# Optimization experiments

Hardware: AMD Instinct MI355X
Metric: run time of the kernel (lower is better)

The kernel has to match this reference:

```python
import jax, jax.numpy as jnp
import numpy as np

N = 50000
E = 800000
F_IN = 64
F_OUT = 64


def setup_inputs() -> dict:
    key = jax.random.key(0)
    ks = jax.random.split(key, 14)
    x = jax.random.normal(ks[0], (N, F_IN), dtype=jnp.float32)
    row_low = jax.random.randint(ks[1], (E,), 0, N)
    col_low = jax.random.randint(ks[2], (E,), 0, N)
    val_low = jax.random.uniform(ks[3], (E,), dtype=jnp.float32)
    row_high = jax.random.randint(ks[4], (E,), 0, N)
    col_high = jax.random.randint(ks[5], (E,), 0, N)
    val_high = jax.random.uniform(ks[6], (E,), dtype=jnp.float32)
    # xavier-uniform style init for weights
    def xavier(k, shape):
        fan_in, fan_out = shape[0], shape[1]
        bound = float(np.sqrt(6.0 / (fan_in + fan_out)))
        return jax.random.uniform(k, shape, jnp.float32, -bound, bound)
    W_low = xavier(ks[7], (F_IN, F_OUT))
    W_high = xavier(ks[8], (F_IN, F_OUT))
    W_mlp = xavier(ks[9], (F_IN, F_OUT))
    a_low = xavier(ks[10], (F_OUT, 1))
    a_high = xavier(ks[11], (F_OUT, 1))
    a_mlp = xavier(ks[12], (F_OUT, 1))
    att3 = xavier(ks[13], (3, 3))
    return dict(x=x, row_low=row_low, col_low=col_low, val_low=val_low,
                row_high=row_high, col_high=col_high, val_high=val_high,
                W_low=W_low, W_high=W_high, W_mlp=W_mlp,
                a_low=a_low, a_high=a_high, a_mlp=a_mlp, att3=att3)


def _spmm(row, col, val, h, n):
    # (sparse adj) @ h : gather source rows, scale by edge weight, scatter-add to dest
    return jax.ops.segment_sum(val[:, None] * h[col], row, num_segments=n)


def reference(x, row_low, col_low, val_low, row_high, col_high, val_high,
              W_low, W_high, W_mlp, a_low, a_high, a_mlp, att3):
    n = x.shape[0]
    out_low = jax.nn.relu(_spmm(row_low, col_low, val_low, x @ W_low, n))
    out_high = jax.nn.relu(_spmm(row_high, col_high, val_high, x @ W_high, n))
    out_mlp = jax.nn.relu(x @ W_mlp)
    T = 3.0
    feats = jnp.concatenate([out_low @ a_low, out_high @ a_high, out_mlp @ a_mlp], axis=1)  # [N,3]
    logits = (jax.nn.sigmoid(feats) @ att3) / T
    att = jax.nn.softmax(logits, axis=1)  # [N,3]
    return 3.0 * (att[:, 0:1] * out_low + att[:, 1:2] * out_high + att[:, 2:3] * out_mlp)
```

## Files before the change

### kernel.cpp

```cpp
#include <hip/hip_runtime.h>


#define NNODE 50000
#define NEDGE 800000
#define NBUCK 782
#define CAP   1300

typedef __attribute__((ext_vector_type(8))) short short8v;
typedef __attribute__((ext_vector_type(4))) float float4v;

__device__ __forceinline__ unsigned short f2bf(float f) {
    unsigned u = __float_as_uint(f);
    u += 0x7FFFu + ((u >> 16) & 1u);
    return (unsigned short)(u >> 16);
}

__global__ __launch_bounds__(256)
void gemm_mfma_kernel(const float* __restrict__ x,
                      const float* __restrict__ Wl, const float* __restrict__ Wh,
                      const float* __restrict__ Wm,
                      unsigned short* __restrict__ hl16,
                      unsigned short* __restrict__ hh16,
                      unsigned short* __restrict__ hm16)
{
    __shared__ unsigned short wt[3][64][72];
    const int t = threadIdx.x;
#pragma unroll 1
    for (int m = 0; m < 3; ++m) {
        const float* __restrict__ W = (m == 0) ? Wl : (m == 1) ? Wh : Wm;
        for (int i = t; i < 4096; i += 256) {
            const int k = i >> 6, c = i & 63;
            wt[m][c][k] = f2bf(W[i]);
        }
    }
    __syncthreads();

    const int wid = t >> 6, lane = t & 63;
    const int node0 = blockIdx.x * 64 + wid * 16;
    if (node0 >= NNODE) return;
    const int arow = lane & 15;
    const int hi = lane >> 4;

    const float* __restrict__ xr = x + (size_t)(node0 + arow) * 64 + hi * 8;
    const float4 pa0 = *(const float4*)(xr + 0);
    const float4 pa1 = *(const float4*)(xr + 4);
    const float4 pb0 = *(const float4*)(xr + 32);
    const float4 pb1 = *(const float4*)(xr + 36);
    short8v a0, a1;
    a0[0] = (short)f2bf(pa0.x); a0[1] = (short)f2bf(pa0.y);
    a0[2] = (short)f2bf(pa0.z); a0[3] = (short)f2bf(pa0.w);
    a0[4] = (short)f2bf(pa1.x); a0[5] = (short)f2bf(pa1.y);
    a0[6] = (short)f2bf(pa1.z); a0[7] = (short)f2bf(pa1.w);
    a1[0] = (short)f2bf(pb0.x); a1[1] = (short)f2bf(pb0.y);
    a1[2] = (short)f2bf(pb0.z); a1[3] = (short)f2bf(pb0.w);
    a1[4] = (short)f2bf(pb1.x); a1[5] = (short)f2bf(pb1.y);
    a1[6] = (short)f2bf(pb1.z); a1[7] = (short)f2bf(pb1.w);

#pragma unroll 1
    for (int m = 0; m < 3; ++m) {
        unsigned short* __restrict__ H = (m == 0) ? hl16 : (m == 1) ? hh16 : hm16;
        float4v acc0 = {0.f, 0.f, 0.f, 0.f}, acc1 = {0.f, 0.f, 0.f, 0.f};
        float4v acc2 = {0.f, 0.f, 0.f, 0.f}, acc3 = {0.f, 0.f, 0.f, 0.f};

#define DO_CT(CT, ACC)                                                          \
        {                                                                       \
            const short8v b0 = *(const short8v*)&wt[m][CT * 16 + arow][hi * 8]; \
            const short8v b1 = *(const short8v*)&wt[m][CT * 16 + arow][32 + hi * 8]; \
            ACC = __builtin_amdgcn_mfma_f32_16x16x32_bf16(a0, b0, ACC, 0, 0, 0); \
            ACC = __builtin_amdgcn_mfma_f32_16x16x32_bf16(a1, b1, ACC, 0, 0, 0); \
        }
        DO_CT(0, acc0) DO_CT(1, acc1) DO_CT(2, acc2) DO_CT(3, acc3)
#undef DO_CT

        const bool rl = (m == 2);
#define ST_CT(CT, ACC)                                                          \
        {                                                                       \
            _Pragma("unroll")                                                   \
            for (int r = 0; r < 4; ++r) {                                       \
                float v = ACC[r];                                               \
                if (rl) v = fmaxf(v, 0.f);                                      \
                H[(size_t)(node0 + hi * 4 + r) * 64 + CT * 16 + arow] = f2bf(v); \
            }                                                                   \
        }
        ST_CT(0, acc0) ST_CT(1, acc1) ST_CT(2, acc2) ST_CT(3, acc3)
#undef ST_CT
    }
}

__global__ __launch_bounds__(512)
void scatter_kernel(const int* __restrict__ row_low, const int* __restrict__ col_low,
                    const float* __restrict__ val_low,
                    const int* __restrict__ row_high, const int* __restrict__ col_high,
                    const float* __restrict__ val_high,
                    unsigned int* __restrict__ gcursor, uint2* __restrict__ packed)
{
    __shared__ unsigned int hist_s[2 * NBUCK];
    __shared__ unsigned int base_s[2 * NBUCK];
    const int t = threadIdx.x;
    const int ebase = blockIdx.x * 8192;

    for (int i = t; i < 2 * NBUCK; i += 512) hist_s[i] = 0u;
    __syncthreads();

    int rows[16]; unsigned int rank[16];
#pragma unroll
    for (int j = 0; j < 16; ++j) {
        const int e = ebase + j * 512 + t;
        rows[j] = 0; rank[j] = 0u;
        if (e < 2 * NEDGE) {
            const int r = (e < NEDGE) ? row_low[e] : row_high[e - NEDGE];
            const int fb = ((e < NEDGE) ? 0 : NBUCK) + (r >> 6);
            rows[j] = r;
            rank[j] = atomicAdd(&hist_s[fb], 1u);
        }
    }
    __syncthreads();
    for (int i = t; i < 2 * NBUCK; i += 512) {
        const unsigned int c = hist_s[i];
        base_s[i] = c ? atomicAdd(&gcursor[i], c) : 0u;
    }
    __syncthreads();
#pragma unroll
    for (int j = 0; j < 16; ++j) {
        const int e = ebase + j * 512 + t;
        if (e < 2 * NEDGE) {
            const int g = (e >= NEDGE);
            const int ee = e - g * NEDGE;
            const int r = rows[j];
            const int c = g ? col_high[ee] : col_low[ee];
            const float v = g ? val_high[ee] : val_low[ee];
            const int fb = g * NBUCK + (r >> 6);
            const unsigned int pos = base_s[fb] + rank[j];
            if (pos < CAP) {
                uint2 pk;
                pk.x = (unsigned int)c | ((unsigned int)(r & 63) << 16);
                pk.y = __float_as_uint(v);
                packed[(size_t)fb * CAP + pos] = pk;
            }
        }
    }
}

__global__ __launch_bounds__(256)
void sort_kernel(uint2* __restrict__ packed,
                 const unsigned int* __restrict__ gcursor,
                 int* __restrict__ rs, int* __restrict__ rc)
{
    __shared__ uint2 es[CAP];
    __shared__ unsigned int hist[64];
    __shared__ unsigned int offs[64];
    __shared__ unsigned int cur[64];

    const int fb = blockIdx.x;
    const int t = threadIdx.x;
    uint2* __restrict__ seg = packed + (size_t)fb * CAP;
    int cnt = (int)gcursor[fb];
    if (cnt > CAP) cnt = CAP;

    if (t < 64) { hist[t] = 0u; cur[t] = 0u; }
    __syncthreads();

    for (int i = t; i < cnt; i += 256) {
        const uint2 p = seg[i];
        es[i] = p;
        atomicAdd(&hist[(p.x >> 16) & 63u], 1u);
    }
    __syncthreads();

    if (t < 64) {
        const int v = (int)hist[t];
        int xsc = v;
#pragma unroll
        for (int d = 1; d < 64; d <<= 1) {
            int y = __shfl_up(xsc, d, 64);
            if (t >= d) xsc += y;
        }
        offs[t] = (unsigned)(xsc - v);
    }
    __syncthreads();

    for (int i = t; i < cnt; i += 256) {
        const uint2 p = es[i];
        const unsigned r = (p.x >> 16) & 63u;
        const unsigned pos = offs[r] + atomicAdd(&cur[r], 1u);
        seg[pos] = p;
    }

    if (t < 64) {
        const int g = (fb >= NBUCK);
        const int node = ((fb - g * NBUCK) << 6) + t;
        if (node < NNODE) {
            rs[g * NNODE + node] = fb * CAP + (int)offs[t];
            rc[g * NNODE + node] = (int)hist[t];
        }
    }
}

#define Q_ISSUE(r0_, r1_, r2_, r3_, rem_, hgp_, U_, V_)                        \
    {                                                                          \
        const unsigned cw = (sub == 0 ? r0_.x : sub == 1 ? r1_.x               \
                             : sub == 2 ? r2_.x : r3_.x);                      \
        const unsigned vb = (sub == 0 ? r0_.y : sub == 1 ? r1_.y               \
                             : sub == 2 ? r2_.y : r3_.y);                      \
        const bool ok = sub < (rem_);                                          \
        const unsigned boff = ok ? ((cw & 0xFFFFu) * 128u + fb2) : fb2;        \
        U_ = *(const uint2*)((const char*)(hgp_) + boff);                      \
        V_ = ok ? __uint_as_float(vb) : 0.f;                                   \
    }

#define Q_FMA(U_, V_, AX_, AY_, AZ_, AW_)                                      \
    {                                                                          \
        AX_ = fmaf(V_, __uint_as_float(U_.x << 16), AX_);                      \
        AY_ = fmaf(V_, __uint_as_float(U_.x & 0xFFFF0000u), AY_);              \
        AZ_ = fmaf(V_, __uint_as_float(U_.y << 16), AZ_);                      \
        AW_ = fmaf(V_, __uint_as_float(U_.y & 0xFFFF0000u), AW_);              \
    }

__global__ __launch_bounds__(256, 4)
void spmm_finalize_kernel(const uint2* __restrict__ packed,
                          const int* __restrict__ rs, const int* __restrict__ rc,
                          const unsigned short* __restrict__ hl16,
                          const unsigned short* __restrict__ hh16,
                          const unsigned short* __restrict__ hm16,
                          const float* __restrict__ aL, const float* __restrict__ aH,
                          const float* __restrict__ aM, const float* __restrict__ att3,
                          float* __restrict__ out)
{
    const int wid = threadIdx.x >> 6;
    const int lane = threadIdx.x & 63;
    const int sub = lane >> 4;
    const int f4 = (lane & 15) << 2;
    const unsigned fb2 = (unsigned)(f4 * 2);
    const int node = blockIdx.x * 4 + wid;
    if (node >= NNODE) return;

    const int sL = __builtin_amdgcn_readfirstlane(rs[node]);
    const int cL = __builtin_amdgcn_readfirstlane(rc[node]);
    const int sH = __builtin_amdgcn_readfirstlane(rs[NNODE + node]);
    const int cH = __builtin_amdgcn_readfirstlane(rc[NNODE + node]);
    const uint2* __restrict__ segL = packed + sL;
    const uint2* __restrict__ segH = packed + sH;
    const int cmax = (cL > cH) ? cL : cH;

    float lx = 0.f, ly = 0.f, lz = 0.f, lw = 0.f;
    float hx = 0.f, hy = 0.f, hz = 0.f, hw = 0.f;

#pragma unroll 1
    for (int i = 0; i < cmax; i += 8) {
        const uint2 l0 = segL[i + 0], l1 = segL[i + 1], l2 = segL[i + 2], l3 = segL[i + 3];
        const uint2 l4 = segL[i + 4], l5 = segL[i + 5], l6 = segL[i + 6], l7 = segL[i + 7];
        const uint2 h0 = segH[i + 0], h1 = segH[i + 1], h2 = segH[i + 2], h3 = segH[i + 3];
        const uint2 h4 = segH[i + 4], h5 = segH[i + 5], h6 = segH[i + 6], h7 = segH[i + 7];
        const int remL = cL - i, remH = cH - i;
        uint2 uL0, uL1, uH0, uH1;
        float vL0, vL1, vH0, vH1;
        Q_ISSUE(l0, l1, l2, l3, remL,     hl16, uL0, vL0);
        Q_ISSUE(l4, l5, l6, l7, remL - 4, hl16, uL1, vL1);
        Q_ISSUE(h0, h1, h2, h3, remH,     hh16, uH0, vH0);
        Q_ISSUE(h4, h5, h6, h7, remH - 4, hh16, uH1, vH1);
        __builtin_amdgcn_sched_barrier(0);
        Q_FMA(uL0, vL0, lx, ly, lz, lw);
        Q_FMA(uL1, vL1, lx, ly, lz, lw);
        Q_FMA(uH0, vH0, hx, hy, hz, hw);
        Q_FMA(uH1, vH1, hx, hy, hz, hw);
    }

    lx += __shfl_xor(lx, 16, 64); ly += __shfl_xor(ly, 16, 64);
    lz += __shfl_xor(lz, 16, 64); lw += __shfl_xor(lw, 16, 64);
    hx += __shfl_xor(hx, 16, 64); hy += __shfl_xor(hy, 16, 64);
    hz += __shfl_xor(hz, 16, 64); hw += __shfl_xor(hw, 16, 64);
    lx += __shfl_xor(lx, 32, 64); ly += __shfl_xor(ly, 32, 64);
    lz += __shfl_xor(lz, 32, 64); lw += __shfl_xor(lw, 32, 64);
    hx += __shfl_xor(hx, 32, 64); hy += __shfl_xor(hy, 32, 64);
    hz += __shfl_xor(hz, 32, 64); hw += __shfl_xor(hw, 32, 64);

    const float olx = fmaxf(lx, 0.f), oly = fmaxf(ly, 0.f);
    const float olz = fmaxf(lz, 0.f), olw = fmaxf(lw, 0.f);
    const float ohx = fmaxf(hx, 0.f), ohy = fmaxf(hy, 0.f);
    const float ohz = fmaxf(hz, 0.f), ohw = fmaxf(hw, 0.f);

    const uint2 om2 = *(const uint2*)&hm16[(size_t)node * 64 + f4];
    const float omx = __uint_as_float(om2.x << 16);
    const float omy = __uint_as_float(om2.x & 0xFFFF0000u);
    const float omz = __uint_as_float(om2.y << 16);
    const float omw = __uint_as_float(om2.y & 0xFFFF0000u);

    const float4 aL4 = *(const float4*)&aL[f4];
    const float4 aH4 = *(const float4*)&aH[f4];
    const float4 aM4 = *(const float4*)&aM[f4];

    float f0 = olx * aL4.x + oly * aL4.y + olz * aL4.z + olw * aL4.w;
    float f1 = ohx * aH4.x + ohy * aH4.y + ohz * aH4.z + ohw * aH4.w;
    float f2 = omx * aM4.x + omy * aM4.y + omz * aM4.z + omw * aM4.w;
#pragma unroll
    for (int msk = 1; msk < 16; msk <<= 1) {
        f0 += __shfl_xor(f0, msk, 64);
        f1 += __shfl_xor(f1, msk, 64);
        f2 += __shfl_xor(f2, msk, 64);
    }
    const float s0 = 1.f / (1.f + __expf(-f0));
    const float s1 = 1.f / (1.f + __expf(-f1));
    const float s2 = 1.f / (1.f + __expf(-f2));
    const float invT = 1.f / 3.f;
    const float l0g = (s0 * att3[0] + s1 * att3[3] + s2 * att3[6]) * invT;
    const float l1g = (s0 * att3[1] + s1 * att3[4] + s2 * att3[7]) * invT;
    const float l2g = (s0 * att3[2] + s1 * att3[5] + s2 * att3[8]) * invT;
    const float mx = fmaxf(l0g, fmaxf(l1g, l2g));
    const float e0 = __expf(l0g - mx);
    const float e1 = __expf(l1g - mx);
    const float e2 = __expf(l2g - mx);
    const float inv = 1.f / (e0 + e1 + e2);
    const float wl = 3.f * inv * e0, wh = 3.f * inv * e1, wm = 3.f * inv * e2;

    if (lane < 16) {
        float4 o;
        o.x = wl * olx + wh * ohx + wm * omx;
        o.y = wl * oly + wh * ohy + wm * omy;
        o.z = wl * olz + wh * ohz + wm * omz;
        o.w = wl * olw + wh * ohw + wm * omw;
        *(float4*)&out[(size_t)node * 64 + f4] = o;
    }
}

extern "C" void kernel_launch(void* const* d_in, const int* in_sizes, int n_in,
                              void* d_out, int out_size, void* d_ws, size_t ws_size,
                              hipStream_t stream)
{
    const float* x        = (const float*)d_in[0];
    const int*   row_low  = (const int*)  d_in[1];
    const int*   col_low  = (const int*)  d_in[2];
    const float* val_low  = (const float*)d_in[3];
    const int*   row_high = (const int*)  d_in[4];
    const int*   col_high = (const int*)  d_in[5];
    const float* val_high = (const float*)d_in[6];
    const float* W_low    = (const float*)d_in[7];
    const float* W_high   = (const float*)d_in[8];
    const float* W_mlp    = (const float*)d_in[9];
    const float* a_low    = (const float*)d_in[10];
    const float* a_high   = (const float*)d_in[11];
    const float* a_mlp    = (const float*)d_in[12];
    const float* att3     = (const float*)d_in[13];
    float* out = (float*)d_out;

    const size_t NM = (size_t)NNODE * 64;

    unsigned short* hl16    = (unsigned short*)d_ws;
    unsigned short* hh16    = hl16 + NM;
    unsigned short* hm16    = hh16 + NM;
    uint2*          packed  = (uint2*)(hm16 + NM);
    unsigned int*   gcursor = (unsigned int*)(packed + (size_t)2 * NBUCK * CAP);
    int*            rs      = (int*)(gcursor + 2 * NBUCK);
    int*            rc      = rs + 2 * NNODE;

    hipMemsetAsync(gcursor, 0, 2 * NBUCK * sizeof(unsigned int), stream);

    scatter_kernel<<<(2 * NEDGE + 8191) / 8192, 512, 0, stream>>>(
        row_low, col_low, val_low, row_high, col_high, val_high, gcursor, packed);

    gemm_mfma_kernel<<<(NNODE + 63) / 64, 256, 0, stream>>>(
        x, W_low, W_high, W_mlp, hl16, hh16, hm16);

    sort_kernel<<<2 * NBUCK, 256, 0, stream>>>(packed, gcursor, rs, rc);

    spmm_finalize_kernel<<<(NNODE + 3) / 4, 256, 0, stream>>>(
        packed, rs, rc, hl16, hh16, hm16, a_low, a_high, a_mlp, att3, out);
}
```

Baseline: 92.34 us.

## Pad per-node edge segments to multiples of eight to simplify SpMM gather loop

The sort kernel now pads each destination node's edge segment to a multiple of eight entries, zero-filling the tail, and stores a quad count instead of a raw edge count. The finalize loop then reads only the one packed entry each 16-lane group needs instead of loading all eight and selecting, which cuts redundant packed loads and selection logic. The launch bound is raised to allow more waves per SIMD, and the memset is replaced with a tiny zero kernel. CAP grows to hold the padding, and entries past CAP are dropped, which risks lost edges for overfull buckets.

```diff
diff --git a/kernel.cpp b/kernel.cpp
--- a/kernel.cpp
+++ b/kernel.cpp
@@ -4,7 +4,7 @@
 #define NNODE 50000
 #define NEDGE 800000
 #define NBUCK 782
-#define CAP   1300
+#define CAP   1552
 
 typedef __attribute__((ext_vector_type(8))) short short8v;
 typedef __attribute__((ext_vector_type(4))) float float4v;
@@ -13,6 +13,13 @@
     unsigned u = __float_as_uint(f);
     u += 0x7FFFu + ((u >> 16) & 1u);
     return (unsigned short)(u >> 16);
+}
+
+__global__ __launch_bounds__(256)
+void zero_kernel(unsigned int* __restrict__ g)
+{
+    const int i = blockIdx.x * 256 + threadIdx.x;
+    if (i < 2 * NBUCK) g[i] = 0u;
 }
 
 __global__ __launch_bounds__(256)
@@ -168,14 +175,14 @@
     __syncthreads();
 
     if (t < 64) {
-        const int v = (int)hist[t];
-        int xsc = v;
+        const int pv = (int)((hist[t] + 7u) & ~7u);
+        int xsc = pv;
 #pragma unroll
         for (int d = 1; d < 64; d <<= 1) {
             int y = __shfl_up(xsc, d, 64);
             if (t >= d) xsc += y;
         }
-        offs[t] = (unsigned)(xsc - v);
+        offs[t] = (unsigned)(xsc - pv);
     }
     __syncthreads();
 
@@ -183,30 +190,29 @@
         const uint2 p = es[i];
         const unsigned r = (p.x >> 16) & 63u;
         const unsigned pos = offs[r] + atomicAdd(&cur[r], 1u);
-        seg[pos] = p;
+        if (pos < CAP) seg[pos] = p;
+    }
+    if (t < 64) {
+        const unsigned b = offs[t] + hist[t];
+        const unsigned e = offs[t] + ((hist[t] + 7u) & ~7u);
+        const uint2 z = {0u, 0u};
+        for (unsigned u = b; u < e && u < CAP; ++u) seg[u] = z;
     }
 
     if (t < 64) {
         const int g = (fb >= NBUCK);
         const int node = ((fb - g * NBUCK) << 6) + t;
         if (node < NNODE) {
+            const unsigned P = (hist[t] + 7u) & ~7u;
+            const int avail = CAP - (int)offs[t];
+            int nq = (int)(P >> 2);
+            int nqa = avail > 0 ? ((avail >> 2) & ~1) : 0;
+            if (nq > nqa) nq = nqa;
             rs[g * NNODE + node] = fb * CAP + (int)offs[t];
-            rc[g * NNODE + node] = (int)hist[t];
-        }
-    }
-}
-
-#define Q_ISSUE(r0_, r1_, r2_, r3_, rem_, hgp_, U_, V_)                        \
-    {                                                                          \
-        const unsigned cw = (sub == 0 ? r0_.x : sub == 1 ? r1_.x               \
-                             : sub == 2 ? r2_.x : r3_.x);                      \
-        const unsigned vb = (sub == 0 ? r0_.y : sub == 1 ? r1_.y               \
-                             : sub == 2 ? r2_.y : r3_.y);                      \
-        const bool ok = sub < (rem_);                                          \
-        const unsigned boff = ok ? ((cw & 0xFFFFu) * 128u + fb2) : fb2;        \
-        U_ = *(const uint2*)((const char*)(hgp_) + boff);                      \
-        V_ = ok ? __uint_as_float(vb) : 0.f;                                   \
-    }
+            rc[g * NNODE + node] = nq;
+        }
+    }
+}
 
 #define Q_FMA(U_, V_, AX_, AY_, AZ_, AW_)                                      \
     {                                                                          \
@@ -216,7 +222,7 @@
         AW_ = fmaf(V_, __uint_as_float(U_.y & 0xFFFF0000u), AW_);              \
     }
 
-__global__ __launch_bounds__(256, 4)
+__global__ __launch_bounds__(256, 8)
 void spmm_finalize_kernel(const uint2* __restrict__ packed,
                           const int* __restrict__ rs, const int* __restrict__ rc,
                           const unsigned short* __restrict__ hl16,
@@ -235,30 +241,31 @@
     if (node >= NNODE) return;
 
     const int sL = __builtin_amdgcn_readfirstlane(rs[node]);
-    const int cL = __builtin_amdgcn_readfirstlane(rc[node]);
+    const int nqL = __builtin_amdgcn_readfirstlane(rc[node]);
     const int sH = __builtin_amdgcn_readfirstlane(rs[NNODE + node]);
-    const int cH = __builtin_amdgcn_readfirstlane(rc[NNODE + node]);
-    const uint2* __restrict__ segL = packed + sL;
-    const uint2* __restrict__ segH = packed + sH;
-    const int cmax = (cL > cH) ? cL : cH;
+    const int nqH = __builtin_amdgcn_readfirstlane(rc[NNODE + node]);
+    const uint2* __restrict__ segL = packed + sL + sub;
+    const uint2* __restrict__ segH = packed + sH + sub;
+    const int nqm = (nqL > nqH) ? nqL : nqH;
 
     float lx = 0.f, ly = 0.f, lz = 0.f, lw = 0.f;
     float hx = 0.f, hy = 0.f, hz = 0.f, hw = 0.f;
 
 #pragma unroll 1
-    for (int i = 0; i < cmax; i += 8) {
-        const uint2 l0 = segL[i + 0], l1 = segL[i + 1], l2 = segL[i + 2], l3 = segL[i + 3];
-        const uint2 l4 = segL[i + 4], l5 = segL[i + 5], l6 = segL[i + 6], l7 = segL[i + 7];
-        const uint2 h0 = segH[i + 0], h1 = segH[i + 1], h2 = segH[i + 2], h3 = segH[i + 3];
-        const uint2 h4 = segH[i + 4], h5 = segH[i + 5], h6 = segH[i + 6], h7 = segH[i + 7];
-        const int remL = cL - i, remH = cH - i;
-        uint2 uL0, uL1, uH0, uH1;
-        float vL0, vL1, vH0, vH1;
-        Q_ISSUE(l0, l1, l2, l3, remL,     hl16, uL0, vL0);
-        Q_ISSUE(l4, l5, l6, l7, remL - 4, hl16, uL1, vL1);
-        Q_ISSUE(h0, h1, h2, h3, remH,     hh16, uH0, vH0);
-        Q_ISSUE(h4, h5, h6, h7, remH - 4, hh16, uH1, vH1);
+    for (int q = 0; q < nqm; q += 2) {
+        const uint2 rL0 = segL[q * 4];
+        const uint2 rL1 = segL[q * 4 + 4];
+        const uint2 rH0 = segH[q * 4];
+        const uint2 rH1 = segH[q * 4 + 4];
+        const uint2 uL0 = *(const uint2*)((const char*)hl16 + (size_t)(((rL0.x & 0xFFFFu) << 7) + fb2));
+        const uint2 uL1 = *(const uint2*)((const char*)hl16 + (size_t)(((rL1.x & 0xFFFFu) << 7) + fb2));
+        const uint2 uH0 = *(const uint2*)((const char*)hh16 + (size_t)(((rH0.x & 0xFFFFu) << 7) + fb2));
+        const uint2 uH1 = *(const uint2*)((const char*)hh16 + (size_t)(((rH1.x & 0xFFFFu) << 7) + fb2));
         __builtin_amdgcn_sched_barrier(0);
+        const float vL0 = (q     < nqL) ? __uint_as_float(rL0.y) : 0.f;
+        const float vL1 = (q + 1 < nqL) ? __uint_as_float(rL1.y) : 0.f;
+        const float vH0 = (q     < nqH) ? __uint_as_float(rH0.y) : 0.f;
+        const float vH1 = (q + 1 < nqH) ? __uint_as_float(rH1.y) : 0.f;
         Q_FMA(uL0, vL0, lx, ly, lz, lw);
         Q_FMA(uL1, vL1, lx, ly, lz, lw);
         Q_FMA(uH0, vH0, hx, hy, hz, hw);
@@ -352,7 +359,7 @@
     int*            rs      = (int*)(gcursor + 2 * NBUCK);
     int*            rc      = rs + 2 * NNODE;
 
-    hipMemsetAsync(gcursor, 0, 2 * NBUCK * sizeof(unsigned int), stream);
+    zero_kernel<<<(2 * NBUCK + 255) / 256, 256, 0, stream>>>(gcursor);
 
     scatter_kernel<<<(2 * NEDGE + 8191) / 8192, 512, 0, stream>>>(
         row_low, col_low, val_low, row_high, col_high, val_high, gcursor, packed);
```

Result: slower. 97.87 us (+6.0%).
